# Performance work log

Hardware: AMD Instinct MI355X
Metric: run time of the kernel (lower is better)

Reference implementation:

```python
import jax, jax.numpy as jnp
import numpy as np

DIM = 1024
HEADS = 16
HEAD_DIM = DIM // HEADS
B, S, L0, L1 = 2, 2048, 2048, 2048


def setup_inputs() -> dict:
    key = jax.random.key(0)
    ks = jax.random.split(key, 10)
    sc = DIM ** -0.5
    return {
        "query": jax.random.normal(ks[0], (B, S, DIM), jnp.float32),
        "l0_keys": jax.random.normal(ks[1], (B, L0, DIM), jnp.float32),
        "l0_values": jax.random.normal(ks[2], (B, L0, DIM), jnp.float32),
        "l1_keys": jax.random.normal(ks[3], (B, L1, DIM), jnp.float32),
        "l1_values": jax.random.normal(ks[4], (B, L1, DIM), jnp.float32),
        "l0_mask": jax.random.randint(ks[5], (S, L0), 0, 2, jnp.int32),
        "Wq": jax.random.normal(ks[6], (DIM, DIM), jnp.float32) * sc,
        "bq": jnp.zeros((DIM,), jnp.float32),
        "Wo": jax.random.normal(ks[7], (DIM, DIM), jnp.float32) * sc,
        "bo": jnp.zeros((DIM,), jnp.float32),
        "gate": jnp.asarray(0.0, jnp.float32),
    }


def reference(query, l0_keys, l0_values, l1_keys, l1_values, l0_mask, Wq, bq, Wo, bo, gate):
    b, s, d = query.shape
    h, hd = HEADS, HEAD_DIM
    scale = hd ** -0.5
    # q: [B,H,S,hd]
    q = (query @ Wq.T + bq).reshape(b, s, h, hd).transpose(0, 2, 1, 3)

    def attend(keys, values, mask):
        L = keys.shape[1]
        k = keys.reshape(b, L, h, hd)
        v = values.reshape(b, L, h, hd)
        scores = jnp.einsum("bhsd,blhd->bhsl", q, k) * scale
        if mask is not None:
            scores = jnp.where(mask[None, None] == 0, -jnp.inf, scores)
        w = jax.nn.softmax(scores, axis=-1)  # [B,H,S,L]
        out = jnp.einsum("bhsl,blhd->bshd", w, v)  # [B,S,H,hd]
        return out, w.mean(axis=1)

    out0, a0 = attend(l0_keys, l0_values, l0_mask)
    out1, a1 = attend(l1_keys, l1_values, None)
    g = jax.nn.sigmoid(gate)
    out = (g * out0 + (1.0 - g) * out1).reshape(b, s, d)
    out = out @ Wo.T + bo
    return out, a0, a1
```

## Files before the change

kernel.cpp:

```cpp
#include <hip/hip_runtime.h>

#define DIM   1024
#define HEADS 16
#define HD    64
#define BB    2
#define SS    2048
#define LLL   2048
#define LOG2E 1.4426950408889634f

typedef __bf16 bf16x8 __attribute__((ext_vector_type(8)));
typedef __bf16 bf16x4v __attribute__((ext_vector_type(4)));
typedef float  f32x4  __attribute__((ext_vector_type(4)));
typedef short  s16x4  __attribute__((ext_vector_type(4)));
typedef unsigned short u16;

static __device__ __forceinline__ u16 f2b(float x) {
  unsigned u = __float_as_uint(x);
  u += 0x7fffu + ((u >> 16) & 1u);
  return (u16)(u >> 16);
}
static __device__ __forceinline__ float b2f(u16 u) {
  return __uint_as_float(((unsigned)u) << 16);
}
static __device__ __forceinline__ f32x4 mfma32(bf16x8 a, bf16x8 b, f32x4 c) {
  return __builtin_amdgcn_mfma_f32_16x16x32_bf16(a, b, c, 0, 0, 0);
}

static __device__ __forceinline__ void gload_lds16(const void* g, void* lds_uniform_base) {
#if __has_builtin(__builtin_amdgcn_global_load_lds)
  __builtin_amdgcn_global_load_lds(
      (const __attribute__((address_space(1))) unsigned int*)g,
      (__attribute__((address_space(3))) unsigned int*)lds_uniform_base, 16, 0, 0);
#else
  const int l = threadIdx.x & 63;
  ((uint4*)lds_uniform_base)[l] = ((const uint4*)g)[0];
#endif
}

__global__ void prep(const float* __restrict__ a, const float* __restrict__ b,
                     const float* __restrict__ c, u16* __restrict__ da,
                     u16* __restrict__ db_, u16* __restrict__ dc,
                     const int* __restrict__ mask, unsigned* __restrict__ mbits,
                     int na4, int nb4, int ncvt) {
  int i = blockIdx.x * blockDim.x + threadIdx.x;
  if (i < ncvt) {
    const float* s; u16* d; int j = i;
    if (j < na4) { s = a; d = da; }
    else if ((j -= na4) < nb4) { s = b; d = db_; }
    else { j -= nb4; s = c; d = dc; }
    float4 f = ((const float4*)s)[j];
    ushort4 o;
    o.x = f2b(f.x); o.y = f2b(f.y); o.z = f2b(f.z); o.w = f2b(f.w);
    ((ushort4*)d)[j] = o;
  } else {
    int j = i - ncvt;
    const int* src = mask + (size_t)j * 32;
    unsigned bm = 0;
#pragma unroll
    for (int jj = 0; jj < 8; ++jj) {
      int4 m = ((const int4*)src)[jj];
      bm |= (m.x != 0 ? 1u : 0u) << (jj * 4 + 0);
      bm |= (m.y != 0 ? 1u : 0u) << (jj * 4 + 1);
      bm |= (m.z != 0 ? 1u : 0u) << (jj * 4 + 2);
      bm |= (m.w != 0 ? 1u : 0u) << (jj * 4 + 3);
    }
    mbits[j] = bm;
  }
}

__global__ __launch_bounds__(256) void pack_k(const float* __restrict__ k0,
                                              const float* __restrict__ k1,
                                              u16* __restrict__ Kfrag) {
  const float SCK = 0.125f * LOG2E;
  const int w = threadIdx.x >> 6, l = threadIdx.x & 63, g = l >> 4, li = l & 15;
  const int lt = blockIdx.x * 4 + w, h = blockIdx.y, z = blockIdx.z;
  const int lay = z >> 1, b = z & 1;
  const float* src = (lay ? k1 : k0) + (size_t)b * LLL * DIM;
  u16* dst = Kfrag + ((((size_t)z * HEADS + h) * 32 + lt) * 8) * 512;
#pragma unroll
  for (int c = 0; c < 8; ++c) {
    int mt = c >> 1, kk = c & 1;
    const float* p = &src[(size_t)(lt * 64 + mt * 16 + li) * DIM + h * 64 + kk * 32 + g * 8];
    float4 f0 = *(const float4*)p;
    float4 f1 = *(const float4*)(p + 4);
    u16 u[8] = {f2b(f0.x * SCK), f2b(f0.y * SCK), f2b(f0.z * SCK), f2b(f0.w * SCK),
                f2b(f1.x * SCK), f2b(f1.y * SCK), f2b(f1.z * SCK), f2b(f1.w * SCK)};
    *(uint4*)&dst[c * 512 + l * 8] = *(uint4*)u;
  }
}

__global__ __launch_bounds__(256) void pack_v(const float* __restrict__ v0,
                                              const float* __restrict__ v1,
                                              u16* __restrict__ Vfrag) {
  __shared__ u16 T[64][72];
  const int lt = blockIdx.x, h = blockIdx.y, z = blockIdx.z;
  const int lay = z >> 1, b = z & 1;
  const float* v = (lay ? v1 : v0) + (size_t)b * LLL * DIM;
  const int t = threadIdx.x;
  {
    int r = t >> 2, c16 = (t & 3) * 16;
    const float* src = &v[(size_t)(lt * 64 + r) * DIM + h * 64 + c16];
#pragma unroll
    for (int i = 0; i < 4; ++i) {
      float4 f = *(const float4*)&src[i * 4];
      T[r][c16 + i * 4 + 0] = f2b(f.x);
      T[r][c16 + i * 4 + 1] = f2b(f.y);
      T[r][c16 + i * 4 + 2] = f2b(f.z);
      T[r][c16 + i * 4 + 3] = f2b(f.w);
    }
  }
  __syncthreads();
  u16* dst = Vfrag + ((((size_t)z * HEADS + h) * 32 + lt) * 8) * 512;
  {
    int lane = t & 63, g = lane >> 4, li = lane & 15;
#pragma unroll
    for (int cc = 0; cc < 2; ++cc) {
      int c = (t >> 6) + cc * 4;
      int pair = c >> 2, dt = c & 3;
      u16 u[8];
#pragma unroll
      for (int j = 0; j < 4; ++j) u[j]     = T[pair * 32 + 4 * g + j][dt * 16 + li];
#pragma unroll
      for (int j = 0; j < 4; ++j) u[4 + j] = T[pair * 32 + 16 + 4 * g + j][dt * 16 + li];
      *(uint4*)&dst[c * 512 + lane * 8] = *(uint4*)u;
    }
  }
}

template<int MODE>
__global__ __launch_bounds__(256) void gemm_nt(const u16* __restrict__ A,
                                               const u16* __restrict__ Bt,
                                               const float* __restrict__ bias,
                                               void* __restrict__ Cv,
                                               int M, int N, int K) {
  __shared__ u16 As[2][128][64];
  __shared__ u16 Bs[2][64][64];
  const int t = threadIdx.x;
  const int w = t >> 6, l = t & 63, g = l >> 4, li = l & 15;
  const int m0 = blockIdx.y * 128, n0 = blockIdx.x * 64;
  const int slotL = w * 64 + l;
  const int rA = slotL >> 3, cA = ((slotL & 7) * 8) ^ ((rA & 7) * 8);

  auto stageAB = [&](int buf, int kt) {
#pragma unroll
    for (int s = 0; s < 4; ++s) {
      int r = rA + s * 32;
      gload_lds16(&A[(size_t)(m0 + r) * K + kt + cA], &As[buf][0][0] + (s * 256 + w * 64) * 8);
    }
#pragma unroll
    for (int s = 0; s < 2; ++s) {
      int r = rA + s * 32;
      gload_lds16(&Bt[(size_t)(n0 + r) * K + kt + cA], &Bs[buf][0][0] + (s * 256 + w * 64) * 8);
    }
  };

  f32x4 acc[2][4] = {};
  stageAB(0, 0);
  __syncthreads();
  int cur = 0;
  for (int kt = 0; kt < K; kt += 64) {
    if (kt + 64 < K) stageAB(cur ^ 1, kt + 64);
#pragma unroll
    for (int kk = 0; kk < 2; ++kk) {
      bf16x8 a[2], bfr[4];
#pragma unroll
      for (int mi = 0; mi < 2; ++mi) {
        int ra = w * 32 + mi * 16 + li;
        a[mi] = *(const bf16x8*)&As[cur][ra][(kk * 32 + g * 8) ^ ((ra & 7) << 3)];
      }
#pragma unroll
      for (int ni = 0; ni < 4; ++ni) {
        int rb = ni * 16 + li;
        bfr[ni] = *(const bf16x8*)&Bs[cur][rb][(kk * 32 + g * 8) ^ ((rb & 7) << 3)];
      }
#pragma unroll
      for (int mi = 0; mi < 2; ++mi)
#pragma unroll
        for (int ni = 0; ni < 4; ++ni)
          acc[mi][ni] = mfma32(a[mi], bfr[ni], acc[mi][ni]);
    }
    __syncthreads();
    cur ^= 1;
  }
#pragma unroll
  for (int mi = 0; mi < 2; ++mi)
#pragma unroll
    for (int ni = 0; ni < 4; ++ni)
#pragma unroll
      for (int v = 0; v < 4; ++v) {
        int rr = m0 + w * 32 + mi * 16 + g * 4 + v;
        int cc = n0 + ni * 16 + li;
        float val = acc[mi][ni][v] + bias[cc];
        if (MODE == 1) {
          ((float*)Cv)[(size_t)rr * N + cc] = val;
        } else {
          int b = rr >> 11, q = rr & 2047;
          int qt = q >> 5, n = (q >> 4) & 1, liq = q & 15;
          int h = (cc >> 6) & 15, kk2 = (cc >> 5) & 1, gp = (cc >> 3) & 3, j = cc & 7;
          size_t base = ((((size_t)b * HEADS + h) * 64 + qt) * 4 + n * 2 + kk2) * 512;
          ((u16*)Cv)[base + (size_t)(gp * 16 + liq) * 8 + j] = f2b(val);
        }
      }
}

template<int MASKED>
static __device__ __forceinline__ void attn_pv_body(int z, int h, int qt, int w, int l,
                                                    const u16* __restrict__ Qfrag,
                                                    const u16* __restrict__ Kfrag,
                                                    const u16* __restrict__ Vfrag,
                                                    const unsigned* __restrict__ mbits,
                                                    u16* __restrict__ out01,
                                                    float* __restrict__ db,
                                                    u16* __restrict__ KV) {
  const int g = l >> 4, li = l & 15;
  const int b = z & 1;
  const u16* kfh = Kfrag + (size_t)(z * HEADS + h) * (32 * 8 * 512);
  const u16* vfh = Vfrag + (size_t)(z * HEADS + h) * (32 * 8 * 512);
  const u16* qfh = Qfrag + (((size_t)(b * HEADS + h) * 64 + qt) * 4) * 512;

  bf16x8 qf[2][2];
#pragma unroll
  for (int n = 0; n < 2; ++n)
#pragma unroll
    for (int kk = 0; kk < 2; ++kk)
      qf[n][kk] = *(const bf16x8*)&qfh[(n * 2 + kk) * 512 + l * 8];

  const unsigned* mrow0 = MASKED ? mbits + (size_t)(qt * 32 + li) * (LLL / 32) : nullptr;
  const unsigned* mrow1 = MASKED ? mrow0 + 16 * (LLL / 32) : nullptr;
  const int shb = 4 * g;
  bf16x8 ones8;
#pragma unroll
  for (int j = 0; j < 8; ++j) ones8[j] = __builtin_bit_cast(__bf16, (u16)0x3F80);

  auto stage = [&](int buf, int lt) {
    const u16* kfl = kfh + (size_t)lt * 4096;
    const u16* vfl = vfh + (size_t)lt * 4096;
#pragma unroll
    for (int i2 = 0; i2 < 2; ++i2) {
      int f = w * 2 + i2;
      const u16* gsrc = (f < 8 ? kfl + f * 512 : vfl + (f - 8) * 512) + l * 8;
      gload_lds16(gsrc, (char*)KV + buf * 16384 + f * 1024);
    }
  };

  f32x4 dacc[2] = {};
  f32x4 oacc[4][2] = {};

  stage(0, 0);
  __syncthreads();
  int cur = 0;
  for (int lt = 0; lt < 32; ++lt) {
    if (lt + 1 < 32) stage(cur ^ 1, lt + 1);
    unsigned mw[2][2];
    if (MASKED) {
      mw[0][0] = mrow0[lt * 2]; mw[0][1] = mrow0[lt * 2 + 1];
      mw[1][0] = mrow1[lt * 2]; mw[1][1] = mrow1[lt * 2 + 1];
    }
    const u16* Ks = KV + cur * 8192;
    const u16* Vs = Ks + 4096;

    auto qk = [&](f32x4 (&s)[2], int mt) {
      bf16x8 k0 = *(const bf16x8*)&Ks[(mt * 2 + 0) * 512 + l * 8];
      bf16x8 k1 = *(const bf16x8*)&Ks[(mt * 2 + 1) * 512 + l * 8];
      f32x4 zz = {};
      __builtin_amdgcn_s_setprio(1);
      s[0] = mfma32(k0, qf[0][0], zz);
      s[0] = mfma32(k1, qf[0][1], s[0]);
      s[1] = mfma32(k0, qf[1][0], zz);
      s[1] = mfma32(k1, qf[1][1], s[1]);
      __builtin_amdgcn_s_setprio(0);
    };
    auto sm = [&](f32x4 (&s)[2], int mt, s16x4 (&wpk)[2]) {
#pragma unroll
      for (int n = 0; n < 2; ++n) {
        unsigned mm = MASKED ? (mw[n][mt >> 1] >> ((mt & 1) * 16 + shb)) : 0u;
        f32x4 ev;
#pragma unroll
        for (int v = 0; v < 4; ++v) {
          float e = __builtin_amdgcn_exp2f(s[n][v]);
          if (MASKED) {
            int spread = ((int)(mm << (31 - v))) >> 31;
            e = __uint_as_float(__float_as_uint(e) & (unsigned)spread);
          }
          ev[v] = e;
        }
        bf16x4v wb = __builtin_convertvector(ev, bf16x4v);
        wpk[n] = __builtin_bit_cast(s16x4, wb);
      }
    };
    auto pv_pair = [&](s16x4 (&w0)[2], s16x4 (&w1)[2], int pair) {
      bf16x8 w8[2];
#pragma unroll
      for (int n = 0; n < 2; ++n) {
        bf16x4v a0 = __builtin_bit_cast(bf16x4v, w0[n]);
        bf16x4v a1 = __builtin_bit_cast(bf16x4v, w1[n]);
        w8[n] = __builtin_shufflevector(a0, a1, 0, 1, 2, 3, 4, 5, 6, 7);
      }
      __builtin_amdgcn_s_setprio(1);
      dacc[0] = mfma32(ones8, w8[0], dacc[0]);
      dacc[1] = mfma32(ones8, w8[1], dacc[1]);
#pragma unroll
      for (int dt = 0; dt < 4; ++dt) {
        bf16x8 vf = *(const bf16x8*)&Vs[(pair * 4 + dt) * 512 + l * 8];
#pragma unroll
        for (int n = 0; n < 2; ++n)
          oacc[dt][n] = mfma32(vf, w8[n], oacc[dt][n]);
      }
      __builtin_amdgcn_s_setprio(0);
    };

    f32x4 sA[2], sB[2];
    s16x4 wA[2], wB[2];
    qk(sA, 0); qk(sB, 1);
    sm(sA, 0, wA);
    qk(sA, 2);
    sm(sB, 1, wB);
    pv_pair(wA, wB, 0);
    qk(sB, 3);
    sm(sA, 2, wA);
    sm(sB, 3, wB);
    pv_pair(wA, wB, 1);
    __syncthreads();
    cur ^= 1;
  }
  float dinv[2];
  dinv[0] = 1.0f / dacc[0][0];
  dinv[1] = 1.0f / dacc[1][0];
  if (l < 16) {
    db[(size_t)(z * HEADS + h) * SS + qt * 32 + li]      = dinv[0];
    db[(size_t)(z * HEADS + h) * SS + qt * 32 + 16 + li] = dinv[1];
  }
  u16* ob = out01 + (size_t)z * SS * DIM;
#pragma unroll
  for (int dt = 0; dt < 4; ++dt)
#pragma unroll
    for (int n = 0; n < 2; ++n) {
      f32x4 o = oacc[dt][n] * dinv[n];
      ushort4 us;
      us.x = f2b(o[0]); us.y = f2b(o[1]); us.z = f2b(o[2]); us.w = f2b(o[3]);
      *(ushort4*)&ob[((size_t)(qt * 32 + n * 16 + li)) * DIM + h * HD + dt * 16 + 4 * g] = us;
    }
}

__global__ __launch_bounds__(512, 4) void attn_pv(const u16* __restrict__ Qfrag,
                                                  const u16* __restrict__ Kfrag,
                                                  const u16* __restrict__ Vfrag,
                                                  const unsigned* __restrict__ mbits,
                                                  u16* __restrict__ out01,
                                                  float* __restrict__ db) {
  __shared__ u16 KV[2][8192];
  const int flat = blockIdx.x;
  const int xcd = flat & 7, i = flat >> 3;
  const int k = i >> 3, qg = i & 7;
  const int zh = xcd + 8 * k;
  const int z = zh >> 4, h = zh & 15;
  const int w = threadIdx.x >> 6, l = threadIdx.x & 63;
  const int qt = qg * 8 + w;
  if (z < 2) attn_pv_body<1>(z, h, qt, w, l, Qfrag, Kfrag, Vfrag, mbits, out01, db, &KV[0][0]);
  else       attn_pv_body<0>(z, h, qt, w, l, Qfrag, Kfrag, Vfrag, mbits, out01, db, &KV[0][0]);
}

template<int MASKED>
static __device__ __forceinline__ void amean_body(int z, int qt, int lt, int w, int l,
                                                  const u16* __restrict__ Qfrag,
                                                  const u16* __restrict__ Kfrag,
                                                  const unsigned* __restrict__ mbits,
                                                  const float* __restrict__ db,
                                                  float* __restrict__ aout,
                                                  u16* __restrict__ KS) {
  const int g = l >> 4, li = l & 15;
  const int b = z & 1;

  const u16* qf_base = Qfrag + (((size_t)(b * HEADS) * 64 + qt) * 4) * 512 + l * 8;
  const float* dbb = db + (size_t)(z * HEADS) * SS + qt * 32 + li;

  auto stageK = [&](int buf, int h) {
    const u16* kfh = Kfrag + ((((size_t)(z * HEADS + h)) * 32 + lt) * 8) * 512;
#pragma unroll
    for (int i2 = 0; i2 < 2; ++i2) {
      int f = w * 2 + i2;
      gload_lds16(kfh + f * 512 + l * 8, (char*)KS + buf * 8192 + f * 1024);
    }
  };

  f32x4 asum[4][2] = {};
  stageK(0, 0);
  __syncthreads();
#pragma unroll 2
  for (int h = 0; h < HEADS; ++h) {
    if (h + 1 < HEADS) stageK((h + 1) & 1, h + 1);
    float dv[2];
    dv[0] = dbb[(size_t)h * SS];
    dv[1] = dbb[(size_t)h * SS + 16];
    bf16x8 qf[2][2];
#pragma unroll
    for (int n = 0; n < 2; ++n)
#pragma unroll
      for (int kk = 0; kk < 2; ++kk)
        qf[n][kk] = *(const bf16x8*)&qf_base[(size_t)h * (64 * 4 * 512) + (n * 2 + kk) * 512];
    const u16* Ks = KS + (h & 1) * 4096;
#pragma unroll
    for (int mt = 0; mt < 4; ++mt) {
      bf16x8 k0 = *(const bf16x8*)&Ks[(mt * 2 + 0) * 512 + l * 8];
      bf16x8 k1 = *(const bf16x8*)&Ks[(mt * 2 + 1) * 512 + l * 8];
#pragma unroll
      for (int n = 0; n < 2; ++n) {
        f32x4 s = {};
        s = mfma32(k0, qf[n][0], s);
        s = mfma32(k1, qf[n][1], s);
#pragma unroll
        for (int v = 0; v < 4; ++v)
          asum[mt][n][v] = __builtin_fmaf(__builtin_amdgcn_exp2f(s[v]), dv[n], asum[mt][n][v]);
      }
    }
    __syncthreads();
  }
  float* ab = aout + (size_t)z * SS * LLL;
#pragma unroll
  for (int mt = 0; mt < 4; ++mt)
#pragma unroll
    for (int n = 0; n < 2; ++n) {
      f32x4 o = asum[mt][n] * 0.0625f;
      if (MASKED) {
        const unsigned* mrow = mbits + (size_t)(qt * 32 + n * 16 + li) * (LLL / 32) + lt * 2;
        unsigned mm = mrow[mt >> 1] >> ((mt & 1) * 16 + 4 * g);
#pragma unroll
        for (int v = 0; v < 4; ++v) {
          int spread = ((int)(mm << (31 - v))) >> 31;
          o[v] = __uint_as_float(__float_as_uint(o[v]) & (unsigned)spread);
        }
      }
      f32x4* dst = (f32x4*)&ab[(size_t)(qt * 32 + n * 16 + li) * LLL + lt * 64 + mt * 16 + 4 * g];
      __builtin_nontemporal_store(o, dst);
    }
}

__global__ __launch_bounds__(256, 4) void amean(const u16* __restrict__ Qfrag,
                                                const u16* __restrict__ Kfrag,
                                                const unsigned* __restrict__ mbits,
                                                const float* __restrict__ db,
                                                float* __restrict__ aout) {
  __shared__ u16 KS[2][4096];
  const int flat = blockIdx.x;
  const int xcd = flat & 7, i = flat >> 3;
  const int k = i >> 4, qg = i & 15;
  const int zlt = xcd + 8 * k;
  const int z = zlt >> 5, lt = zlt & 31;
  const int w = threadIdx.x >> 6, l = threadIdx.x & 63;
  const int qt = qg * 4 + w;
  if (z < 2) amean_body<1>(z, qt, lt, w, l, Qfrag, Kfrag, mbits, db, aout, &KS[0][0]);
  else       amean_body<0>(z, qt, lt, w, l, Qfrag, Kfrag, mbits, db, aout, &KS[0][0]);
}

__global__ void merge_kernel(const u16* __restrict__ o01,
                             const float* __restrict__ gate,
                             u16* __restrict__ merged) {
  int i = blockIdx.x * blockDim.x + threadIdx.x;
  float gv = gate[0];
  float g = 1.0f / (1.0f + __builtin_amdgcn_exp2f(-gv * LOG2E));
  const size_t n = (size_t)BB * SS * DIM;
  ushort4 a = ((const ushort4*)o01)[i];
  ushort4 c = ((const ushort4*)(o01 + n))[i];
  ushort4 o;
  o.x = f2b(g * b2f(a.x) + (1.f - g) * b2f(c.x));
  o.y = f2b(g * b2f(a.y) + (1.f - g) * b2f(c.y));
  o.z = f2b(g * b2f(a.z) + (1.f - g) * b2f(c.z));
  o.w = f2b(g * b2f(a.w) + (1.f - g) * b2f(c.w));
  ((ushort4*)merged)[i] = o;
}

extern "C" void kernel_launch(void* const* d_in, const int* in_sizes, int n_in,
                              void* d_out, int out_size, void* d_ws, size_t ws_size,
                              hipStream_t stream) {
  const float* query = (const float*)d_in[0];
  const float* k0f   = (const float*)d_in[1];
  const float* v0f   = (const float*)d_in[2];
  const float* k1f   = (const float*)d_in[3];
  const float* v1f   = (const float*)d_in[4];
  const int*   mask  = (const int*)d_in[5];
  const float* Wqf   = (const float*)d_in[6];
  const float* bq    = (const float*)d_in[7];
  const float* Wof   = (const float*)d_in[8];
  const float* bo    = (const float*)d_in[9];
  const float* gate  = (const float*)d_in[10];
  float* out = (float*)d_out;

  const size_t nQ = (size_t)BB * SS * DIM;
  const size_t nW = (size_t)DIM * DIM;

  char* ws = (char*)d_ws;
  size_t off = 0;
  auto alloc = [&](size_t bytes) -> char* {
    char* p = ws + off;
    off += (bytes + 255) & ~(size_t)255;
    return p;
  };
  u16*      queryb  = (u16*)alloc(nQ * 2);
  u16*      wqb     = (u16*)alloc(nW * 2);
  u16*      wob     = (u16*)alloc(nW * 2);
  u16*      Qfrag   = (u16*)alloc(nQ * 2);
  u16*      Kfrag   = (u16*)alloc((size_t)2 * nQ * 2);
  u16*      Vfrag   = (u16*)alloc((size_t)2 * nQ * 2);
  unsigned* mbits   = (unsigned*)alloc((size_t)SS * (LLL / 32) * 4);
  float*    db      = (float*)alloc((size_t)4 * HEADS * SS * 4);
  u16*      out01   = (u16*)alloc((size_t)2 * nQ * 2);
  u16*      mergedb = queryb;

  {
    int na4 = (int)(nQ / 4), nb4 = (int)(nW / 4);
    int ncvt = na4 + 2 * nb4;
    int nmask = SS * (LLL / 32);
    prep<<<dim3((ncvt + nmask) / 256), dim3(256), 0, stream>>>(
        query, Wqf, Wof, queryb, wqb, wob, mask, mbits, na4, nb4, ncvt);
  }

  pack_k<<<dim3(LLL / 64 / 4, HEADS, 4), dim3(256), 0, stream>>>(k0f, k1f, Kfrag);
  pack_v<<<dim3(LLL / 64, HEADS, 4), dim3(256), 0, stream>>>(v0f, v1f, Vfrag);

  gemm_nt<2><<<dim3(DIM / 64, (BB * SS) / 128), dim3(256), 0, stream>>>(
      queryb, wqb, bq, (void*)Qfrag, BB * SS, DIM, DIM);

  attn_pv<<<dim3(512), dim3(512), 0, stream>>>(Qfrag, Kfrag, Vfrag, mbits, out01, db);

  amean<<<dim3(2048), dim3(256), 0, stream>>>(Qfrag, Kfrag, mbits, db, out + nQ);

  merge_kernel<<<dim3((int)(nQ / 4 / 256)), dim3(256), 0, stream>>>(out01, gate, mergedb);

  gemm_nt<1><<<dim3(DIM / 64, (BB * SS) / 128), dim3(256), 0, stream>>>(
      mergedb, wob, bo, (void*)out, BB * SS, DIM, DIM);
}
```

Measured before the change: 209.1 us.

## Split attention key range across two wave groups per block with LDS reduction

The attention-PV kernel now runs 1024 threads per block. Two groups of 8 waves each process half of the key tiles for the same query tiles, each group with its own double-buffered LDS staging. Partial softmax denominators and output accumulators are then reduced through LDS before normalisation and store. This raises parallelism and latency hiding per block, at the cost of extra barriers, reduction traffic and more LDS per block, which may reduce co-resident blocks. The reduction sums raw exponentials without a running max, which relies on the existing softmax formulation not using a per-split max.

```diff
diff --git a/kernel.cpp b/kernel.cpp
--- a/kernel.cpp
+++ b/kernel.cpp
@@ -204,19 +204,20 @@
 }
 
 template<int MASKED>
-static __device__ __forceinline__ void attn_pv_body(int z, int h, int qt, int w, int l,
+static __device__ __forceinline__ void attn_pv_body(int z, int h, int qt, int g2, int wg, int l,
                                                     const u16* __restrict__ Qfrag,
                                                     const u16* __restrict__ Kfrag,
                                                     const u16* __restrict__ Vfrag,
                                                     const unsigned* __restrict__ mbits,
                                                     u16* __restrict__ out01,
                                                     float* __restrict__ db,
-                                                    u16* __restrict__ KV) {
+                                                    u16* __restrict__ KVall) {
   const int g = l >> 4, li = l & 15;
   const int b = z & 1;
   const u16* kfh = Kfrag + (size_t)(z * HEADS + h) * (32 * 8 * 512);
   const u16* vfh = Vfrag + (size_t)(z * HEADS + h) * (32 * 8 * 512);
   const u16* qfh = Qfrag + (((size_t)(b * HEADS + h) * 64 + qt) * 4) * 512;
+  u16* KV = KVall + (size_t)g2 * 16384;
 
   bf16x8 qf[2][2];
 #pragma unroll
@@ -237,7 +238,7 @@
     const u16* vfl = vfh + (size_t)lt * 4096;
 #pragma unroll
     for (int i2 = 0; i2 < 2; ++i2) {
-      int f = w * 2 + i2;
+      int f = wg * 2 + i2;
       const u16* gsrc = (f < 8 ? kfl + f * 512 : vfl + (f - 8) * 512) + l * 8;
       gload_lds16(gsrc, (char*)KV + buf * 16384 + f * 1024);
     }
@@ -246,11 +247,13 @@
   f32x4 dacc[2] = {};
   f32x4 oacc[4][2] = {};
 
-  stage(0, 0);
+  const int lt0 = g2 * 16;
+  stage(0, lt0);
   __syncthreads();
   int cur = 0;
-  for (int lt = 0; lt < 32; ++lt) {
-    if (lt + 1 < 32) stage(cur ^ 1, lt + 1);
+  for (int it = 0; it < 16; ++it) {
+    const int lt = lt0 + it;
+    if (it + 1 < 16) stage(cur ^ 1, lt + 1);
     unsigned mw[2][2];
     if (MASKED) {
       mw[0][0] = mrow0[lt * 2]; mw[0][1] = mrow0[lt * 2 + 1];
@@ -323,41 +326,77 @@
     __syncthreads();
     cur ^= 1;
   }
-  float dinv[2];
-  dinv[0] = 1.0f / dacc[0][0];
-  dinv[1] = 1.0f / dacc[1][0];
-  if (l < 16) {
-    db[(size_t)(z * HEADS + h) * SS + qt * 32 + li]      = dinv[0];
-    db[(size_t)(z * HEADS + h) * SS + qt * 32 + 16 + li] = dinv[1];
-  }
-  u16* ob = out01 + (size_t)z * SS * DIM;
-#pragma unroll
-  for (int dt = 0; dt < 4; ++dt)
-#pragma unroll
-    for (int n = 0; n < 2; ++n) {
-      f32x4 o = oacc[dt][n] * dinv[n];
-      ushort4 us;
-      us.x = f2b(o[0]); us.y = f2b(o[1]); us.z = f2b(o[2]); us.w = f2b(o[3]);
-      *(ushort4*)&ob[((size_t)(qt * 32 + n * 16 + li)) * DIM + h * HD + dt * 16 + 4 * g] = us;
-    }
-}
-
-__global__ __launch_bounds__(512, 4) void attn_pv(const u16* __restrict__ Qfrag,
-                                                  const u16* __restrict__ Kfrag,
-                                                  const u16* __restrict__ Vfrag,
-                                                  const unsigned* __restrict__ mbits,
-                                                  u16* __restrict__ out01,
-                                                  float* __restrict__ db) {
-  __shared__ u16 KV[2][8192];
+
+  float* X = (float*)KVall;
+  const int slot = (wg * 64 + l) * 4;
+  if (g2 == 1) {
+    *(f32x4*)&X[0 * 2048 + slot] = dacc[0];
+    *(f32x4*)&X[1 * 2048 + slot] = dacc[1];
+    *(f32x4*)&X[2 * 2048 + slot] = oacc[0][0];
+    *(f32x4*)&X[3 * 2048 + slot] = oacc[0][1];
+    *(f32x4*)&X[4 * 2048 + slot] = oacc[1][0];
+    *(f32x4*)&X[5 * 2048 + slot] = oacc[1][1];
+  }
+  __syncthreads();
+  if (g2 == 0) {
+    dacc[0]    += *(const f32x4*)&X[0 * 2048 + slot];
+    dacc[1]    += *(const f32x4*)&X[1 * 2048 + slot];
+    oacc[0][0] += *(const f32x4*)&X[2 * 2048 + slot];
+    oacc[0][1] += *(const f32x4*)&X[3 * 2048 + slot];
+    oacc[1][0] += *(const f32x4*)&X[4 * 2048 + slot];
+    oacc[1][1] += *(const f32x4*)&X[5 * 2048 + slot];
+  }
+  __syncthreads();
+  if (g2 == 1) {
+    *(f32x4*)&X[0 * 2048 + slot] = oacc[2][0];
+    *(f32x4*)&X[1 * 2048 + slot] = oacc[2][1];
+    *(f32x4*)&X[2 * 2048 + slot] = oacc[3][0];
+    *(f32x4*)&X[3 * 2048 + slot] = oacc[3][1];
+  }
+  __syncthreads();
+  if (g2 == 0) {
+    oacc[2][0] += *(const f32x4*)&X[0 * 2048 + slot];
+    oacc[2][1] += *(const f32x4*)&X[1 * 2048 + slot];
+    oacc[3][0] += *(const f32x4*)&X[2 * 2048 + slot];
+    oacc[3][1] += *(const f32x4*)&X[3 * 2048 + slot];
+
+    float dinv[2];
+    dinv[0] = 1.0f / dacc[0][0];
+    dinv[1] = 1.0f / dacc[1][0];
+    if (l < 16) {
+      db[(size_t)(z * HEADS + h) * SS + qt * 32 + li]      = dinv[0];
+      db[(size_t)(z * HEADS + h) * SS + qt * 32 + 16 + li] = dinv[1];
+    }
+    u16* ob = out01 + (size_t)z * SS * DIM;
+#pragma unroll
+    for (int dt = 0; dt < 4; ++dt)
+#pragma unroll
+      for (int n = 0; n < 2; ++n) {
+        f32x4 o = oacc[dt][n] * dinv[n];
+        ushort4 us;
+        us.x = f2b(o[0]); us.y = f2b(o[1]); us.z = f2b(o[2]); us.w = f2b(o[3]);
+        *(ushort4*)&ob[((size_t)(qt * 32 + n * 16 + li)) * DIM + h * HD + dt * 16 + 4 * g] = us;
+      }
+  }
+}
+
+__global__ __launch_bounds__(1024, 8) void attn_pv(const u16* __restrict__ Qfrag,
+                                                   const u16* __restrict__ Kfrag,
+                                                   const u16* __restrict__ Vfrag,
+                                                   const unsigned* __restrict__ mbits,
+                                                   u16* __restrict__ out01,
+                                                   float* __restrict__ db) {
+  __shared__ u16 KV[2][2][8192];
   const int flat = blockIdx.x;
   const int xcd = flat & 7, i = flat >> 3;
   const int k = i >> 3, qg = i & 7;
   const int zh = xcd + 8 * k;
   const int z = zh >> 4, h = zh & 15;
   const int w = threadIdx.x >> 6, l = threadIdx.x & 63;
-  const int qt = qg * 8 + w;
-  if (z < 2) attn_pv_body<1>(z, h, qt, w, l, Qfrag, Kfrag, Vfrag, mbits, out01, db, &KV[0][0]);
-  else       attn_pv_body<0>(z, h, qt, w, l, Qfrag, Kfrag, Vfrag, mbits, out01, db, &KV[0][0]);
+  const int g2 = w >> 3, wg = w & 7;
+  const int qt = qg * 8 + wg;
+  if (z < 2) attn_pv_body<1>(z, h, qt, g2, wg, l, Qfrag, Kfrag, Vfrag, mbits, out01, db, &KV[0][0][0]);
+  else       attn_pv_body<0>(z, h, qt, g2, wg, l, Qfrag, Kfrag, Vfrag, mbits, out01, db, &KV[0][0][0]);
 }
 
 template<int MASKED>
@@ -520,7 +559,7 @@
   gemm_nt<2><<<dim3(DIM / 64, (BB * SS) / 128), dim3(256), 0, stream>>>(
       queryb, wqb, bq, (void*)Qfrag, BB * SS, DIM, DIM);
 
-  attn_pv<<<dim3(512), dim3(512), 0, stream>>>(Qfrag, Kfrag, Vfrag, mbits, out01, db);
+  attn_pv<<<dim3(512), dim3(1024), 0, stream>>>(Qfrag, Kfrag, Vfrag, mbits, out01, db);
 
   amean<<<dim3(2048), dim3(256), 0, stream>>>(Qfrag, Kfrag, mbits, db, out + nQ);
 
```

New measurement: 833.9 us. 3.99x slower.
